# Kernel tuning notes

Measured on AMD Instinct MI355X. Metric: run time of the kernel, lower is better.

Reference implementation:

```python
import jax, jax.numpy as jnp
import numpy as np

H = 1024      # hidden_size
NH = 16       # num heads
HD = H // NH  # head dim


def setup_inputs() -> dict:
    key = jax.random.key(0)
    ks = jax.random.split(key, 10)
    s = 1.0 / np.sqrt(H)
    return {
        "hidden_states": jax.random.normal(ks[0], (2, 2048, H), jnp.float32),
        "attention_mask": jnp.zeros((2, 1, 1, 2048), jnp.float32),
        "Wq": jax.random.uniform(ks[1], (H, H), jnp.float32, -s, s),
        "bq": jnp.zeros((H,), jnp.float32),
        "Wk": jax.random.uniform(ks[2], (H, H), jnp.float32, -s, s),
        "bk": jnp.zeros((H,), jnp.float32),
        "Wv": jax.random.uniform(ks[3], (H, H), jnp.float32, -s, s),
        "bv": jnp.zeros((H,), jnp.float32),
        "Wo": jax.random.uniform(ks[4], (H, H), jnp.float32, -s, s),
        "bo": jnp.zeros((H,), jnp.float32),
    }


def _split_heads(x):
    b, s, _ = x.shape
    return x.reshape(b, s, NH, HD).transpose(0, 2, 1, 3)  # [B,NH,S,HD]


def reference(hidden_states, attention_mask, Wq, bq, Wk, bk, Wv, bv, Wo, bo):
    q = _split_heads(hidden_states @ Wq.T + bq)
    k = _split_heads(hidden_states @ Wk.T + bk)
    v = _split_heads(hidden_states @ Wv.T + bv)
    scores = jnp.einsum("bhqd,bhkd->bhqk", q, k) / np.sqrt(HD)
    scores = scores + attention_mask
    probs = jax.nn.softmax(scores, axis=-1)  # dropout prob=0 / eval mode -> no-op
    ctx = jnp.einsum("bhqk,bhkd->bhqd", probs, v)
    b, _, s, _ = ctx.shape
    ctx = ctx.transpose(0, 2, 1, 3).reshape(b, s, H)
    return ctx @ Wo.T + bo
```

## Files before the change

kernel.cpp:

```cpp
#include <hip/hip_runtime.h>
#include <hip/hip_bf16.h>

typedef __bf16 bf16_t;
typedef __bf16 bf16x8 __attribute__((ext_vector_type(8)));
typedef float f32x4 __attribute__((ext_vector_type(4)));
typedef float f32x16 __attribute__((ext_vector_type(16)));
typedef unsigned short u16;

#define DEVI __device__ __forceinline__
#define MFMA16x16x32(A, B, C) __builtin_amdgcn_mfma_f32_16x16x32_bf16(A, B, C, 0, 0, 0)
#define MFMA32x32x16(A, B, C) __builtin_amdgcn_mfma_f32_32x32x16_bf16(A, B, C, 0, 0, 0)

DEVI void gload_lds16(const void* g, void* l) {
  __builtin_amdgcn_global_load_lds(
      (const __attribute__((address_space(1))) void*)g,
      (__attribute__((address_space(3))) void*)l, 16, 0, 0);
}

DEVI u16 bits_of(bf16_t x) { return __builtin_bit_cast(u16, x); }

DEVI unsigned pk2(float lo, float hi) {
  return (unsigned)bits_of((bf16_t)lo) | ((unsigned)bits_of((bf16_t)hi) << 16);
}

DEVI bf16x8 mk_frag(unsigned s0, unsigned s1, unsigned s2, unsigned s3) {
  int4 t;
  t.x = (int)s0; t.y = (int)s1; t.z = (int)s2; t.w = (int)s3;
  return __builtin_bit_cast(bf16x8, t);
}

__global__ void cvt_f32_bf16(const float4* __restrict__ in, ushort4* __restrict__ out, int n4) {
  int i = blockIdx.x * 256 + threadIdx.x;
  if (i < n4) {
    float4 v = in[i];
    ushort4 o;
    o.x = bits_of((bf16_t)v.x);
    o.y = bits_of((bf16_t)v.y);
    o.z = bits_of((bf16_t)v.z);
    o.w = bits_of((bf16_t)v.w);
    out[i] = o;
  }
}

template <int OUT_KIND>
__global__ __launch_bounds__(256, 3) void gemm_bt(
    const bf16_t* __restrict__ A,
    const bf16_t* __restrict__ W0, const bf16_t* __restrict__ W1, const bf16_t* __restrict__ W2,
    const float* __restrict__ b0, const float* __restrict__ b1, const float* __restrict__ b2,
    void* o0, void* o1, void* o2) {
  constexpr int K = 1024, N = 1024;
  const int z = blockIdx.z;
  const bf16_t* W = (z == 0) ? W0 : ((z == 1) ? W1 : W2);
  const float* bias = (z == 0) ? b0 : ((z == 1) ? b1 : b2);
  void* out = (z == 0) ? o0 : ((z == 1) ? o1 : o2);

  __shared__ bf16_t As[128 * 32];
  __shared__ bf16_t Bs[128 * 32];

  const int tid = threadIdx.x;
  const int wave = tid >> 6, lane = tid & 63;
  const int g = lane >> 4, l15 = lane & 15;
  const long m0 = (long)blockIdx.x * 128;
  const long n0 = (long)blockIdx.y * 128;

  const int srow = lane >> 2;
  const int scol = (lane & 3) * 8;

  const int wr = (wave >> 1) * 64;
  const int wc = (wave & 1) * 64;

  f32x4 acc[4][4] = {};

  for (int k0 = 0; k0 < K; k0 += 32) {
    __syncthreads();
#pragma unroll
    for (int t = 0; t < 2; ++t) {
      int chunk = wave * 2 + t;
      int row = chunk * 16 + srow;
      gload_lds16(A + (m0 + row) * K + k0 + scol, (char*)As + chunk * 1024);
      gload_lds16(W + (n0 + row) * K + k0 + scol, (char*)Bs + chunk * 1024);
    }
    __syncthreads();

    bf16x8 af[4], bfr[4];
#pragma unroll
    for (int i = 0; i < 4; ++i)
      af[i] = *(const bf16x8*)(As + (wr + i * 16 + l15) * 32 + g * 8);
#pragma unroll
    for (int i = 0; i < 4; ++i)
      bfr[i] = *(const bf16x8*)(Bs + (wc + i * 16 + l15) * 32 + g * 8);
#pragma unroll
    for (int mi = 0; mi < 4; ++mi)
#pragma unroll
      for (int ni = 0; ni < 4; ++ni)
        acc[mi][ni] = MFMA16x16x32(af[mi], bfr[ni], acc[mi][ni]);
  }

#pragma unroll
  for (int ni = 0; ni < 4; ++ni) {
    long col = n0 + wc + ni * 16 + l15;
    float bv = bias[col];
#pragma unroll
    for (int mi = 0; mi < 4; ++mi) {
#pragma unroll
      for (int r = 0; r < 4; ++r) {
        long row = m0 + wr + mi * 16 + g * 4 + r;
        float v = acc[mi][ni][r] + bv;
        if (OUT_KIND == 0)
          ((bf16_t*)out)[row * N + col] = (bf16_t)v;
        else
          ((float*)out)[row * N + col] = v;
      }
    }
  }
}

__global__ __launch_bounds__(128, 2) void attn_fwd2(
    const bf16_t* __restrict__ Qm, const bf16_t* __restrict__ Km,
    const bf16_t* __restrict__ Vm, const float* __restrict__ mask,
    bf16_t* __restrict__ ctx) {
  constexpr int S = 2048, Hs = 1024;
  int id = blockIdx.y * 32 + blockIdx.x;
  int swz = ((id & 7) << 7) | (id >> 3);
  const int qb = swz & 31;
  const int bh = swz >> 5;
  const int b = bh >> 4, h = bh & 15;

  const int tid = threadIdx.x;
  const int wave = tid >> 6, lane = tid & 63;
  const int l31 = lane & 31, hi = lane >> 5;

  __shared__ bf16_t Kb_[2][64 * 64];
  __shared__ bf16_t Vb_[2][64 * 64];
  __shared__ float Ms[2048];

  const char* Kg = (const char*)(Km + ((long)b * S) * Hs + h * 64);
  const bf16_t* Vg = Vm + ((long)b * S) * Hs + h * 64;
  const float* mrow = mask + b * S;

  const long qrow = (long)b * S + qb * 64 + wave * 32 + l31;
  const bf16_t* Qr = Qm + qrow * Hs + h * 64 + hi * 8;
  bf16x8 qB[4];
#pragma unroll
  for (int ks = 0; ks < 4; ++ks) qB[ks] = *(const bf16x8*)(Qr + ks * 16);

  const int ka = tid & 15, dq = tid >> 4;
  const bf16_t* Vsrc0 = Vg + (long)(4 * ka) * Hs + dq * 8;

  const int krow_in8 = lane >> 3;
  const int kslot = (lane & 7) ^ krow_in8;

#pragma unroll
  for (int c = 0; c < 4; ++c) {
    int ch = wave * 4 + c;
    gload_lds16((const char*)mrow + ch * 1024 + lane * 16, (char*)Ms + ch * 1024);
  }
#pragma unroll
  for (int c = 0; c < 4; ++c) {
    int ch = wave * 4 + c;
    gload_lds16(Kg + (long)(ch * 8 + krow_in8) * (Hs * 2) + kslot * 16,
                (char*)Kb_[0] + ch * 1024);
  }
  int4 v0 = *(const int4*)(Vsrc0);
  int4 v1 = *(const int4*)(Vsrc0 + Hs);
  int4 v2 = *(const int4*)(Vsrc0 + 2 * Hs);
  int4 v3 = *(const int4*)(Vsrc0 + 3 * Hs);
  {
    const u16* p0 = (const u16*)&v0; const u16* p1 = (const u16*)&v1;
    const u16* p2 = (const u16*)&v2; const u16* p3 = (const u16*)&v3;
#pragma unroll
    for (int j = 0; j < 8; ++j) {
      int d = dq * 8 + j;
      int2 w;
      w.x = (int)((unsigned)p0[j] | ((unsigned)p1[j] << 16));
      w.y = (int)((unsigned)p2[j] | ((unsigned)p3[j] << 16));
      *(int2*)((char*)Vb_[0] + d * 128 + ((8 * ka) ^ (j << 4))) = w;
    }
  }
  __syncthreads();

  f32x16 acc0 = {}, acc1 = {};
  float mrun = -1e30f, lrun = 0.0f;

  for (int t = 0; t < 32; ++t) {
    const int cur = t & 1;
    const char* kb_c = (const char*)Kb_[cur];
    const char* vb_c = (const char*)Vb_[cur];

    if (t < 31) {
      const bf16_t* Vs = Vsrc0 + (long)((t + 1) * 64) * Hs;
      v0 = *(const int4*)(Vs);
      v1 = *(const int4*)(Vs + Hs);
      v2 = *(const int4*)(Vs + 2 * Hs);
      v3 = *(const int4*)(Vs + 3 * Hs);
#pragma unroll
      for (int c = 0; c < 4; ++c) {
        int ch = wave * 4 + c;
        gload_lds16(Kg + (long)((t + 1) * 64 + ch * 8 + krow_in8) * (Hs * 2) + kslot * 16,
                    (char*)Kb_[cur ^ 1] + ch * 1024);
      }
    }

    f32x16 sc0 = {}, sc1 = {};
#pragma unroll
    for (int ks = 0; ks < 4; ++ks) {
      bf16x8 kf = *(const bf16x8*)(kb_c + l31 * 128 + (((2 * ks + hi) * 16) ^ ((l31 & 7) << 4)));
      sc0 = MFMA32x32x16(kf, qB[ks], sc0);
    }
#pragma unroll
    for (int ks = 0; ks < 4; ++ks) {
      int row = 32 + l31;
      bf16x8 kf = *(const bf16x8*)(kb_c + row * 128 + (((2 * ks + hi) * 16) ^ ((row & 7) << 4)));
      sc1 = MFMA32x32x16(kf, qB[ks], sc1);
    }

    const float* mbase = Ms + t * 64;
    float mt = -1e30f;
#pragma unroll
    for (int st = 0; st < 2; ++st) {
      f32x16& s = st ? sc1 : sc0;
#pragma unroll
      for (int rg = 0; rg < 4; ++rg) {
        f32x4 mk = *(const f32x4*)(mbase + st * 32 + rg * 8 + hi * 4);
#pragma unroll
        for (int i = 0; i < 4; ++i) {
          float v = s[rg * 4 + i] * 0.125f + mk[i];
          s[rg * 4 + i] = v;
          mt = fmaxf(mt, v);
        }
      }
    }
    mt = fmaxf(mt, __shfl_xor(mt, 32, 64));

    bool defer = __all(mt <= mrun + 8.0f);
    if (!defer) {
      float mnew = fmaxf(mrun, mt);
      float fct = __expf(mrun - mnew);
      lrun *= fct;
#pragma unroll
      for (int i = 0; i < 16; ++i) { acc0[i] *= fct; acc1[i] *= fct; }
      mrun = mnew;
    }
    float ls = 0.0f;
#pragma unroll
    for (int st = 0; st < 2; ++st) {
      f32x16& s = st ? sc1 : sc0;
#pragma unroll
      for (int i = 0; i < 16; ++i) {
        float p = __expf(s[i] - mrun);
        s[i] = p;
        ls += p;
      }
    }
    ls += __shfl_xor(ls, 32, 64);
    lrun += ls;

    if (t < 31) {
      const u16* p0 = (const u16*)&v0; const u16* p1 = (const u16*)&v1;
      const u16* p2 = (const u16*)&v2; const u16* p3 = (const u16*)&v3;
      char* vb_n = (char*)Vb_[cur ^ 1];
#pragma unroll
      for (int j = 0; j < 8; ++j) {
        int d = dq * 8 + j;
        int2 w;
        w.x = (int)((unsigned)p0[j] | ((unsigned)p1[j] << 16));
        w.y = (int)((unsigned)p2[j] | ((unsigned)p3[j] << 16));
        *(int2*)(vb_n + d * 128 + ((8 * ka) ^ (j << 4))) = w;
      }
    }

#pragma unroll
    for (int st = 0; st < 2; ++st) {
      f32x16& s = st ? sc1 : sc0;
      unsigned a0 = pk2(s[0], s[1]),   b0 = pk2(s[4], s[5]);
      unsigned a1 = pk2(s[2], s[3]),   b1 = pk2(s[6], s[7]);
      unsigned a2 = pk2(s[8], s[9]),   b2 = pk2(s[12], s[13]);
      unsigned a3 = pk2(s[10], s[11]), b3 = pk2(s[14], s[15]);
      asm("v_permlane32_swap_b32 %0, %1" : "+v"(a0), "+v"(b0));
      asm("v_permlane32_swap_b32 %0, %1" : "+v"(a1), "+v"(b1));
      asm("v_permlane32_swap_b32 %0, %1" : "+v"(a2), "+v"(b2));
      asm("v_permlane32_swap_b32 %0, %1" : "+v"(a3), "+v"(b3));
      bf16x8 pb0 = mk_frag(a0, a1, b0, b1);
      bf16x8 pb1 = mk_frag(a2, a3, b2, b3);
#pragma unroll
      for (int ks2 = 0; ks2 < 2; ++ks2) {
        bf16x8 pb = ks2 ? pb1 : pb0;
        int slot = st * 4 + ks2 * 2 + hi;
#pragma unroll
        for (int dh = 0; dh < 2; ++dh) {
          int d = dh * 32 + l31;
          bf16x8 va = *(const bf16x8*)(vb_c + d * 128 + ((slot * 16) ^ ((d & 7) << 4)));
          if (dh == 0) acc0 = MFMA32x32x16(va, pb, acc0);
          else         acc1 = MFMA32x32x16(va, pb, acc1);
        }
      }
    }
    __syncthreads();
  }

  float inv = 1.0f / lrun;
  bf16_t* cb = ctx + qrow * Hs + h * 64;
#pragma unroll
  for (int dh = 0; dh < 2; ++dh) {
    f32x16& a = dh ? acc1 : acc0;
#pragma unroll
    for (int rg = 0; rg < 4; ++rg) {
      ushort4 o;
      o.x = bits_of((bf16_t)(a[rg * 4 + 0] * inv));
      o.y = bits_of((bf16_t)(a[rg * 4 + 1] * inv));
      o.z = bits_of((bf16_t)(a[rg * 4 + 2] * inv));
      o.w = bits_of((bf16_t)(a[rg * 4 + 3] * inv));
      *(ushort4*)(cb + dh * 32 + rg * 8 + hi * 4) = o;
    }
  }
}

extern "C" void kernel_launch(void* const* d_in, const int* in_sizes, int n_in,
                              void* d_out, int out_size, void* d_ws, size_t ws_size,
                              hipStream_t stream) {
  (void)in_sizes; (void)n_in; (void)out_size; (void)ws_size;
  const float* X  = (const float*)d_in[0];
  const float* mask = (const float*)d_in[1];
  const float* Wq = (const float*)d_in[2];
  const float* bq = (const float*)d_in[3];
  const float* Wk = (const float*)d_in[4];
  const float* bk = (const float*)d_in[5];
  const float* Wv = (const float*)d_in[6];
  const float* bv = (const float*)d_in[7];
  const float* Wo = (const float*)d_in[8];
  const float* bo = (const float*)d_in[9];

  char* ws = (char*)d_ws;
  bf16_t* Xb  = (bf16_t*)(ws + 0);
  bf16_t* Wqb = (bf16_t*)(ws + 8388608);
  bf16_t* Wkb = (bf16_t*)(ws + 10485760);
  bf16_t* Wvb = (bf16_t*)(ws + 12582912);
  bf16_t* Wob = (bf16_t*)(ws + 14680064);
  bf16_t* Qb  = (bf16_t*)(ws + 16777216);
  bf16_t* Kb  = (bf16_t*)(ws + 25165824);
  bf16_t* Vb  = (bf16_t*)(ws + 33554432);
  bf16_t* Cb  = (bf16_t*)(ws + 41943040);

  cvt_f32_bf16<<<4096, 256, 0, stream>>>((const float4*)X,  (ushort4*)Xb,  1048576);
  cvt_f32_bf16<<<1024, 256, 0, stream>>>((const float4*)Wq, (ushort4*)Wqb, 262144);
  cvt_f32_bf16<<<1024, 256, 0, stream>>>((const float4*)Wk, (ushort4*)Wkb, 262144);
  cvt_f32_bf16<<<1024, 256, 0, stream>>>((const float4*)Wv, (ushort4*)Wvb, 262144);
  cvt_f32_bf16<<<1024, 256, 0, stream>>>((const float4*)Wo, (ushort4*)Wob, 262144);

  dim3 gq(32, 8, 3);
  gemm_bt<0><<<gq, 256, 0, stream>>>(Xb, Wqb, Wkb, Wvb, bq, bk, bv, Qb, Kb, Vb);

  dim3 ga(32, 32, 1);
  attn_fwd2<<<ga, 128, 0, stream>>>(Qb, Kb, Vb, mask, Cb);

  dim3 go(32, 8, 1);
  gemm_bt<1><<<go, 256, 0, stream>>>(Cb, Wob, Wob, Wob, bo, bo, bo, d_out, d_out, d_out);
}
```

Measured before the change: 140.8 us.

## Split attention over two KV halves with merge kernel, fold scale into Q

Attention now splits the key sequence into two halves across a third grid dimension, doubling the block count. Each half writes unnormalized bf16 partial outputs plus row sum/max, and a new merge kernel combines them. The softmax scale and log2(e) are folded into the Q projection epilogue so exp2 can be used directly, and the mask is read from global memory instead of staged in LDS. The five conversion launches become one kernel. The cost is an extra launch and a partial-output round trip, plus bf16 rounding of the unnormalized partials.

```diff
diff --git a/kernel.cpp b/kernel.cpp
--- a/kernel.cpp
+++ b/kernel.cpp
@@ -29,17 +29,33 @@
   return __builtin_bit_cast(bf16x8, t);
 }
 
-__global__ void cvt_f32_bf16(const float4* __restrict__ in, ushort4* __restrict__ out, int n4) {
+#if __has_builtin(__builtin_amdgcn_exp2f)
+DEVI float exp2_fast(float x) { return __builtin_amdgcn_exp2f(x); }
+#else
+DEVI float exp2_fast(float x) { return __exp2f(x); }
+#endif
+
+__global__ void cvt_all(const float4* __restrict__ X,
+                        const float4* __restrict__ Wq, const float4* __restrict__ Wk,
+                        const float4* __restrict__ Wv, const float4* __restrict__ Wo,
+                        ushort4* __restrict__ out) {
   int i = blockIdx.x * 256 + threadIdx.x;
-  if (i < n4) {
-    float4 v = in[i];
-    ushort4 o;
-    o.x = bits_of((bf16_t)v.x);
-    o.y = bits_of((bf16_t)v.y);
-    o.z = bits_of((bf16_t)v.z);
-    o.w = bits_of((bf16_t)v.w);
-    out[i] = o;
-  }
+  const float4* src;
+  int off;
+  if (i < 1048576) { src = X; off = i; }
+  else {
+    int j = i - 1048576;
+    int seg = j >> 18;
+    off = j & 262143;
+    src = (seg == 0) ? Wq : (seg == 1) ? Wk : (seg == 2) ? Wv : Wo;
+  }
+  float4 v = src[off];
+  ushort4 o;
+  o.x = bits_of((bf16_t)v.x);
+  o.y = bits_of((bf16_t)v.y);
+  o.z = bits_of((bf16_t)v.z);
+  o.w = bits_of((bf16_t)v.w);
+  out[i] = o;
 }
 
 template <int OUT_KIND>
@@ -47,12 +63,13 @@
     const bf16_t* __restrict__ A,
     const bf16_t* __restrict__ W0, const bf16_t* __restrict__ W1, const bf16_t* __restrict__ W2,
     const float* __restrict__ b0, const float* __restrict__ b1, const float* __restrict__ b2,
-    void* o0, void* o1, void* o2) {
+    void* o0, void* o1, void* o2, float s0, float s1, float s2) {
   constexpr int K = 1024, N = 1024;
   const int z = blockIdx.z;
   const bf16_t* W = (z == 0) ? W0 : ((z == 1) ? W1 : W2);
   const float* bias = (z == 0) ? b0 : ((z == 1) ? b1 : b2);
   void* out = (z == 0) ? o0 : ((z == 1) ? o1 : o2);
+  const float scale = (z == 0) ? s0 : ((z == 1) ? s1 : s2);
 
   __shared__ bf16_t As[128 * 32];
   __shared__ bf16_t Bs[128 * 32];
@@ -105,7 +122,7 @@
 #pragma unroll
       for (int r = 0; r < 4; ++r) {
         long row = m0 + wr + mi * 16 + g * 4 + r;
-        float v = acc[mi][ni][r] + bv;
+        float v = (acc[mi][ni][r] + bv) * scale;
         if (OUT_KIND == 0)
           ((bf16_t*)out)[row * N + col] = (bf16_t)v;
         else
@@ -115,16 +132,19 @@
   }
 }
 
-__global__ __launch_bounds__(128, 2) void attn_fwd2(
+__global__ __launch_bounds__(128, 2) void attn_fwd3(
     const bf16_t* __restrict__ Qm, const bf16_t* __restrict__ Km,
     const bf16_t* __restrict__ Vm, const float* __restrict__ mask,
-    bf16_t* __restrict__ ctx) {
+    bf16_t* __restrict__ P0, bf16_t* __restrict__ P1, float2* __restrict__ lr) {
   constexpr int S = 2048, Hs = 1024;
-  int id = blockIdx.y * 32 + blockIdx.x;
-  int swz = ((id & 7) << 7) | (id >> 3);
+  constexpr float L2E = 1.4426950408889634f;
+  int id = (blockIdx.z * 32 + blockIdx.y) * 32 + blockIdx.x;
+  int swz = ((id & 7) << 8) | (id >> 3);
   const int qb = swz & 31;
-  const int bh = swz >> 5;
+  const int bh = (swz >> 5) & 31;
+  const int split = swz >> 10;
   const int b = bh >> 4, h = bh & 15;
+  const int koff = split * 1024;
 
   const int tid = threadIdx.x;
   const int wave = tid >> 6, lane = tid & 63;
@@ -132,11 +152,10 @@
 
   __shared__ bf16_t Kb_[2][64 * 64];
   __shared__ bf16_t Vb_[2][64 * 64];
-  __shared__ float Ms[2048];
-
-  const char* Kg = (const char*)(Km + ((long)b * S) * Hs + h * 64);
-  const bf16_t* Vg = Vm + ((long)b * S) * Hs + h * 64;
-  const float* mrow = mask + b * S;
+
+  const char* Kg = (const char*)(Km + ((long)b * S + koff) * Hs + h * 64);
+  const bf16_t* Vg = Vm + ((long)b * S + koff) * Hs + h * 64;
+  const float* mrow = mask + b * S + koff;
 
   const long qrow = (long)b * S + qb * 64 + wave * 32 + l31;
   const bf16_t* Qr = Qm + qrow * Hs + h * 64 + hi * 8;
@@ -150,11 +169,6 @@
   const int krow_in8 = lane >> 3;
   const int kslot = (lane & 7) ^ krow_in8;
 
-#pragma unroll
-  for (int c = 0; c < 4; ++c) {
-    int ch = wave * 4 + c;
-    gload_lds16((const char*)mrow + ch * 1024 + lane * 16, (char*)Ms + ch * 1024);
-  }
 #pragma unroll
   for (int c = 0; c < 4; ++c) {
     int ch = wave * 4 + c;
@@ -180,14 +194,14 @@
   __syncthreads();
 
   f32x16 acc0 = {}, acc1 = {};
-  float mrun = -1e30f, lrun = 0.0f;
-
-  for (int t = 0; t < 32; ++t) {
+  float rho = 0.0f, lrun = 0.0f;
+
+  for (int t = 0; t < 16; ++t) {
     const int cur = t & 1;
     const char* kb_c = (const char*)Kb_[cur];
     const char* vb_c = (const char*)Vb_[cur];
 
-    if (t < 31) {
+    if (t < 15) {
       const bf16_t* Vs = Vsrc0 + (long)((t + 1) * 64) * Hs;
       v0 = *(const int4*)(Vs);
       v1 = *(const int4*)(Vs + Hs);
@@ -200,6 +214,12 @@
                     (char*)Kb_[cur ^ 1] + ch * 1024);
       }
     }
+    float4 mk[8];
+#pragma unroll
+    for (int st = 0; st < 2; ++st)
+#pragma unroll
+      for (int rg = 0; rg < 4; ++rg)
+        mk[st * 4 + rg] = *(const float4*)(mrow + t * 64 + st * 32 + rg * 8 + hi * 4);
 
     f32x16 sc0 = {}, sc1 = {};
 #pragma unroll
@@ -214,48 +234,56 @@
       sc1 = MFMA32x32x16(kf, qB[ks], sc1);
     }
 
-    const float* mbase = Ms + t * 64;
-    float mt = -1e30f;
+    float m4[4] = {-1e30f, -1e30f, -1e30f, -1e30f};
 #pragma unroll
     for (int st = 0; st < 2; ++st) {
       f32x16& s = st ? sc1 : sc0;
 #pragma unroll
       for (int rg = 0; rg < 4; ++rg) {
-        f32x4 mk = *(const f32x4*)(mbase + st * 32 + rg * 8 + hi * 4);
+        float4 m = mk[st * 4 + rg];
 #pragma unroll
         for (int i = 0; i < 4; ++i) {
-          float v = s[rg * 4 + i] * 0.125f + mk[i];
+          float v = fmaf(((const float*)&m)[i], L2E, s[rg * 4 + i]);
           s[rg * 4 + i] = v;
-          mt = fmaxf(mt, v);
+          m4[i] = fmaxf(m4[i], v);
         }
       }
     }
+    float mt = fmaxf(fmaxf(m4[0], m4[1]), fmaxf(m4[2], m4[3]));
     mt = fmaxf(mt, __shfl_xor(mt, 32, 64));
 
-    bool defer = __all(mt <= mrun + 8.0f);
-    if (!defer) {
-      float mnew = fmaxf(mrun, mt);
-      float fct = __expf(mrun - mnew);
+    if (!__all(mt - rho <= 24.0f)) {
+      float mw = mt;
+#pragma unroll
+      for (int off = 1; off < 32; off <<= 1) mw = fmaxf(mw, __shfl_xor(mw, off, 64));
+      float fct = exp2_fast(rho - mw);
       lrun *= fct;
 #pragma unroll
       for (int i = 0; i < 16; ++i) { acc0[i] *= fct; acc1[i] *= fct; }
-      mrun = mnew;
-    }
-    float ls = 0.0f;
+      rho = mw;
+    }
+    float rho_u = __builtin_amdgcn_readfirstlane(rho);
+    if (rho_u != 0.0f) {
+#pragma unroll
+      for (int i = 0; i < 16; ++i) { sc0[i] -= rho_u; sc1[i] -= rho_u; }
+    }
+
+    float s4[4] = {0.f, 0.f, 0.f, 0.f};
 #pragma unroll
     for (int st = 0; st < 2; ++st) {
       f32x16& s = st ? sc1 : sc0;
 #pragma unroll
       for (int i = 0; i < 16; ++i) {
-        float p = __expf(s[i] - mrun);
+        float p = exp2_fast(s[i]);
         s[i] = p;
-        ls += p;
-      }
-    }
+        s4[i & 3] += p;
+      }
+    }
+    float ls = (s4[0] + s4[1]) + (s4[2] + s4[3]);
     ls += __shfl_xor(ls, 32, 64);
     lrun += ls;
 
-    if (t < 31) {
+    if (t < 15) {
       const u16* p0 = (const u16*)&v0; const u16* p1 = (const u16*)&v1;
       const u16* p2 = (const u16*)&v2; const u16* p3 = (const u16*)&v3;
       char* vb_n = (char*)Vb_[cur ^ 1];
@@ -298,21 +326,46 @@
     __syncthreads();
   }
 
-  float inv = 1.0f / lrun;
-  bf16_t* cb = ctx + qrow * Hs + h * 64;
+  bf16_t* Psel = split ? P1 : P0;
+  bf16_t* pb = Psel + qrow * Hs + h * 64;
 #pragma unroll
   for (int dh = 0; dh < 2; ++dh) {
     f32x16& a = dh ? acc1 : acc0;
 #pragma unroll
     for (int rg = 0; rg < 4; ++rg) {
       ushort4 o;
-      o.x = bits_of((bf16_t)(a[rg * 4 + 0] * inv));
-      o.y = bits_of((bf16_t)(a[rg * 4 + 1] * inv));
-      o.z = bits_of((bf16_t)(a[rg * 4 + 2] * inv));
-      o.w = bits_of((bf16_t)(a[rg * 4 + 3] * inv));
-      *(ushort4*)(cb + dh * 32 + rg * 8 + hi * 4) = o;
-    }
-  }
+      o.x = bits_of((bf16_t)a[rg * 4 + 0]);
+      o.y = bits_of((bf16_t)a[rg * 4 + 1]);
+      o.z = bits_of((bf16_t)a[rg * 4 + 2]);
+      o.w = bits_of((bf16_t)a[rg * 4 + 3]);
+      *(ushort4*)(pb + dh * 32 + rg * 8 + hi * 4) = o;
+    }
+  }
+  if (hi == 0)
+    lr[split * 65536 + bh * 2048 + qb * 64 + wave * 32 + l31] = make_float2(lrun, rho);
+}
+
+__global__ void attn_merge(const bf16_t* __restrict__ P0, const bf16_t* __restrict__ P1,
+                           const float2* __restrict__ lr, bf16_t* __restrict__ ctx) {
+  int i = blockIdx.x * 256 + threadIdx.x;
+  int row = i >> 7;
+  int g8 = i & 127;
+  int h = g8 >> 3;
+  int b = row >> 11, q = row & 2047;
+  int bh = b * 16 + h;
+  float2 l0 = lr[bh * 2048 + q];
+  float2 l1 = lr[65536 + bh * 2048 + q];
+  float M = fmaxf(l0.y, l1.y);
+  float w0 = exp2_fast(l0.y - M), w1 = exp2_fast(l1.y - M);
+  float inv = 1.0f / (l0.x * w0 + l1.x * w1);
+  w0 *= inv; w1 *= inv;
+  bf16x8 a0 = ((const bf16x8*)P0)[i];
+  bf16x8 a1 = ((const bf16x8*)P1)[i];
+  u16 o[8];
+#pragma unroll
+  for (int j = 0; j < 8; ++j)
+    o[j] = bits_of((bf16_t)((float)a0[j] * w0 + (float)a1[j] * w1));
+  ((int4*)ctx)[i] = *(const int4*)o;
 }
 
 extern "C" void kernel_launch(void* const* d_in, const int* in_sizes, int n_in,
@@ -340,19 +393,23 @@
   bf16_t* Kb  = (bf16_t*)(ws + 25165824);
   bf16_t* Vb  = (bf16_t*)(ws + 33554432);
   bf16_t* Cb  = (bf16_t*)(ws + 41943040);
-
-  cvt_f32_bf16<<<4096, 256, 0, stream>>>((const float4*)X,  (ushort4*)Xb,  1048576);
-  cvt_f32_bf16<<<1024, 256, 0, stream>>>((const float4*)Wq, (ushort4*)Wqb, 262144);
-  cvt_f32_bf16<<<1024, 256, 0, stream>>>((const float4*)Wk, (ushort4*)Wkb, 262144);
-  cvt_f32_bf16<<<1024, 256, 0, stream>>>((const float4*)Wv, (ushort4*)Wvb, 262144);
-  cvt_f32_bf16<<<1024, 256, 0, stream>>>((const float4*)Wo, (ushort4*)Wob, 262144);
-
+  bf16_t* P0  = (bf16_t*)(ws + 50331648);
+  bf16_t* P1  = (bf16_t*)(ws + 58720256);
+  float2* lrb = (float2*)(ws + 67108864);
+
+  cvt_all<<<8192, 256, 0, stream>>>((const float4*)X, (const float4*)Wq, (const float4*)Wk,
+                                    (const float4*)Wv, (const float4*)Wo, (ushort4*)Xb);
+
+  const float QSCALE = 0.125f * 1.4426950408889634f;
   dim3 gq(32, 8, 3);
-  gemm_bt<0><<<gq, 256, 0, stream>>>(Xb, Wqb, Wkb, Wvb, bq, bk, bv, Qb, Kb, Vb);
-
-  dim3 ga(32, 32, 1);
-  attn_fwd2<<<ga, 128, 0, stream>>>(Qb, Kb, Vb, mask, Cb);
+  gemm_bt<0><<<gq, 256, 0, stream>>>(Xb, Wqb, Wkb, Wvb, bq, bk, bv, Qb, Kb, Vb,
+                                     QSCALE, 1.0f, 1.0f);
+
+  dim3 ga(32, 32, 2);
+  attn_fwd3<<<ga, 128, 0, stream>>>(Qb, Kb, Vb, mask, P0, P1, lrb);
+  attn_merge<<<2048, 256, 0, stream>>>(P0, P1, lrb, Cb);
 
   dim3 go(32, 8, 1);
-  gemm_bt<1><<<go, 256, 0, stream>>>(Cb, Wob, Wob, Wob, bo, bo, bo, d_out, d_out, d_out);
-}
+  gemm_bt<1><<<go, 256, 0, stream>>>(Cb, Wob, Wob, Wob, bo, bo, bo, d_out, d_out, d_out,
+                                     1.0f, 1.0f, 1.0f);
+}
```

Result: slower. 169.8 us (+20.6%).
